# Kernel optimization log

Measured on AMD Instinct MI355X. Metric: run time of the kernel, lower is better.

Reference implementation:

```python
import jax, jax.numpy as jnp
import numpy as np

N = 1024
X_DIM = 128
Y_DIM = 128
HIDDEN = 256


def setup_inputs() -> dict:
    key = jax.random.key(0)
    ks = jax.random.split(key, 6)
    x_samples = jax.random.normal(ks[0], (N, X_DIM), dtype=jnp.float32)
    y_samples = jax.random.normal(ks[1], (N, Y_DIM), dtype=jnp.float32)
    in_dim = X_DIM + Y_DIM
    # Linear params (kaiming-uniform-ish small init)
    W1 = jax.random.normal(ks[2], (in_dim, HIDDEN), dtype=jnp.float32) / np.sqrt(in_dim)
    b1 = jnp.zeros((HIDDEN,), dtype=jnp.float32)
    W2 = jax.random.normal(ks[3], (HIDDEN, 1), dtype=jnp.float32) / np.sqrt(HIDDEN)
    b2 = jnp.zeros((1,), dtype=jnp.float32)
    return {"x_samples": x_samples, "y_samples": y_samples,
            "W1": W1, "b1": b1, "W2": W2, "b2": b2}


def reference(x_samples, y_samples, W1, b1, W2, b2):
    n = y_samples.shape[0]
    W1x, W1y = W1[:X_DIM], W1[X_DIM:]
    xp = x_samples @ W1x          # [N, H]  (x_tile[i, j] = x[j])
    yp = y_samples @ W1y          # [N, H]  (y_tile[i, j] = y[i])
    # T0: F(cat([x_i, y_i])) on the diagonal pairs -> [N, 1]
    T0 = jax.nn.relu(xp + yp + b1) @ W2 + b2
    # T1: F over all pairs (i, j) -> [N, N, 1]
    h = jax.nn.relu(yp[:, None, :] + xp[None, :, :] + b1)   # [N, N, H]
    T1 = h @ W2 + b2                                        # [N, N, 1]
    lse = jax.scipy.special.logsumexp(T1, axis=1)           # [N, 1] over dim=1
    lower_bound = T0.mean() - (lse.mean() - jnp.log(jnp.float32(n)))
    return lower_bound
```

## Files before the change

### kernel.cpp

```cpp
#include <hip/hip_runtime.h>

#define N_SAMP 1024
#define XD     128
#define HID    256


__global__ __launch_bounds__(256) void gemm_xy(
    const float* __restrict__ x, const float* __restrict__ y,
    const float* __restrict__ W1, const float* __restrict__ b1,
    float* __restrict__ xpbT, float* __restrict__ ypT,
    float* __restrict__ S, float* __restrict__ T0sum)
{
    const int k  = threadIdx.x;
    const int r0 = blockIdx.x * 4;

    if (threadIdx.x < 4) S[blockIdx.x * 4 + threadIdx.x] = 0.f;
    if (blockIdx.x == 0 && threadIdx.x == 4) T0sum[0] = 0.f;

    float ax0 = 0.f, ax1 = 0.f, ax2 = 0.f, ax3 = 0.f;
    float ay0 = 0.f, ay1 = 0.f, ay2 = 0.f, ay3 = 0.f;

    #pragma unroll 4
    for (int d = 0; d < XD; ++d) {
        const float wx = W1[d * HID + k];
        const float wy = W1[(XD + d) * HID + k];
        ax0 = fmaf(x[(r0 + 0) * XD + d], wx, ax0);
        ax1 = fmaf(x[(r0 + 1) * XD + d], wx, ax1);
        ax2 = fmaf(x[(r0 + 2) * XD + d], wx, ax2);
        ax3 = fmaf(x[(r0 + 3) * XD + d], wx, ax3);
        ay0 = fmaf(y[(r0 + 0) * XD + d], wy, ay0);
        ay1 = fmaf(y[(r0 + 1) * XD + d], wy, ay1);
        ay2 = fmaf(y[(r0 + 2) * XD + d], wy, ay2);
        ay3 = fmaf(y[(r0 + 3) * XD + d], wy, ay3);
    }

    const float bk = b1[k];
    float4 xs = make_float4(ax0 + bk, ax1 + bk, ax2 + bk, ax3 + bk);
    float4 ys = make_float4(ay0, ay1, ay2, ay3);
    *(float4*)&xpbT[k * N_SAMP + r0] = xs;
    *(float4*)&ypT [k * N_SAMP + r0] = ys;
}

__global__ __launch_bounds__(128) void pair_lse(
    const float* __restrict__ ypT, const float* __restrict__ xpbT,
    const float* __restrict__ W2,
    float* __restrict__ S, float* __restrict__ T0sum)
{
    __shared__ float yl[HID * 32];

    const int tid = threadIdx.x;
    const int tj  = tid & 15;
    const int ti  = tid >> 4;
    const int jb  = blockIdx.x * 64;
    const int ib  = blockIdx.y * 32;
    const int j0  = jb + tj * 4;
    const int i0  = ib + ti * 4;

    #pragma unroll
    for (int s = 0; s < 16; ++s) {
        const int f  = s * 128 + tid;
        const int k  = f >> 3;
        const int iq = (f & 7) * 4;
        *(float4*)&yl[k * 32 + iq] =
            *(const float4*)&ypT[k * N_SAMP + ib + iq];
    }
    __syncthreads();

    float acc[4][4];
    #pragma unroll
    for (int a = 0; a < 4; ++a)
        #pragma unroll
        for (int b = 0; b < 4; ++b) acc[a][b] = 0.f;

    const int ti4 = ti * 4;

    #pragma unroll 8
    for (int k = 0; k < HID; ++k) {
        const float4 xv = *(const float4*)&xpbT[k * N_SAMP + j0];
        const float4 yv = *(const float4*)&yl[k * 32 + ti4];
        const float  w  = W2[k];
        const float xs[4] = {xv.x, xv.y, xv.z, xv.w};
        const float ys[4] = {yv.x, yv.y, yv.z, yv.w};
        #pragma unroll
        for (int a = 0; a < 4; ++a)
            #pragma unroll
            for (int b = 0; b < 4; ++b)
                acc[a][b] = fmaf(fmaxf(ys[a] + xs[b], 0.f), w, acc[a][b]);
    }

    #pragma unroll
    for (int a = 0; a < 4; ++a) {
        float e = __expf(acc[a][0]) + __expf(acc[a][1])
                + __expf(acc[a][2]) + __expf(acc[a][3]);
        #pragma unroll
        for (int off = 8; off; off >>= 1) e += __shfl_xor(e, off, 16);
        if (tj == 0) atomicAdd(&S[i0 + a], e);
    }

    if ((int)blockIdx.x == (int)(blockIdx.y >> 1)) {
        float dv = 0.f;
        #pragma unroll
        for (int a = 0; a < 4; ++a) {
            const int dd = i0 + a - j0;
            float t = 0.f;
            if      (dd == 0) t = acc[a][0];
            else if (dd == 1) t = acc[a][1];
            else if (dd == 2) t = acc[a][2];
            else if (dd == 3) t = acc[a][3];
            dv += t;
        }
        #pragma unroll
        for (int off = 32; off; off >>= 1) dv += __shfl_xor(dv, off, 64);
        if ((tid & 63) == 0) atomicAdd(T0sum, dv);
    }
}

__global__ __launch_bounds__(256) void finalize(
    const float* __restrict__ S, const float* __restrict__ T0sum,
    const float* __restrict__ b2, float* __restrict__ out)
{
    __shared__ float red[4];
    const int tid = threadIdx.x;

    float ls = 0.f;
    for (int i = tid; i < N_SAMP; i += 256) ls += logf(S[i]);
    #pragma unroll
    for (int off = 32; off; off >>= 1) ls += __shfl_xor(ls, off, 64);
    if ((tid & 63) == 0) red[tid >> 6] = ls;
    __syncthreads();

    if (tid == 0) {
        const float lse_sum = red[0] + red[1] + red[2] + red[3];
        const float t0_mean  = T0sum[0] / (float)N_SAMP + b2[0];
        const float lse_mean = lse_sum / (float)N_SAMP + b2[0] - logf((float)N_SAMP);
        out[0] = t0_mean - lse_mean;
    }
}

extern "C" void kernel_launch(void* const* d_in, const int* in_sizes, int n_in,
                              void* d_out, int out_size, void* d_ws, size_t ws_size,
                              hipStream_t stream)
{
    const float* x  = (const float*)d_in[0];
    const float* y  = (const float*)d_in[1];
    const float* W1 = (const float*)d_in[2];
    const float* b1 = (const float*)d_in[3];
    const float* W2 = (const float*)d_in[4];
    const float* b2 = (const float*)d_in[5];

    float* ws   = (float*)d_ws;
    float* S    = ws;
    float* T0s  = ws + 1024;
    float* xpbT = ws + 2048;
    float* ypT  = ws + 2048 + HID * N_SAMP;

    gemm_xy <<<dim3(N_SAMP / 4), dim3(256), 0, stream>>>(x, y, W1, b1,
                                                         xpbT, ypT, S, T0s);
    pair_lse<<<dim3(16, 32),     dim3(128), 0, stream>>>(ypT, xpbT, W2, S, T0s);
    finalize<<<dim3(1),          dim3(256), 0, stream>>>(S, T0s, b2, (float*)d_out);
}
```

Baseline: 120.5 us.

## Split hidden dimension across blocks, stage both operands in LDS, add row LSE kernel

Result: no change. 122.5 us (+1.7%).

```diff
diff --git a/kernel.cpp b/kernel.cpp
--- a/kernel.cpp
+++ b/kernel.cpp
@@ -3,19 +3,19 @@
 #define N_SAMP 1024
 #define XD     128
 #define HID    256
+#define KHALF  128
 
 
 __global__ __launch_bounds__(256) void gemm_xy(
     const float* __restrict__ x, const float* __restrict__ y,
     const float* __restrict__ W1, const float* __restrict__ b1,
     float* __restrict__ xpbT, float* __restrict__ ypT,
-    float* __restrict__ S, float* __restrict__ T0sum)
+    float* __restrict__ T0sum)
 {
     const int k  = threadIdx.x;
     const int r0 = blockIdx.x * 4;
 
-    if (threadIdx.x < 4) S[blockIdx.x * 4 + threadIdx.x] = 0.f;
-    if (blockIdx.x == 0 && threadIdx.x == 4) T0sum[0] = 0.f;
+    if (blockIdx.x == 0 && threadIdx.x == 0) T0sum[0] = 0.f;
 
     float ax0 = 0.f, ax1 = 0.f, ax2 = 0.f, ax3 = 0.f;
     float ay0 = 0.f, ay1 = 0.f, ay2 = 0.f, ay3 = 0.f;
@@ -41,28 +41,27 @@
     *(float4*)&ypT [k * N_SAMP + r0] = ys;
 }
 
-__global__ __launch_bounds__(128) void pair_lse(
+__global__ __launch_bounds__(256) void pair_partial(
     const float* __restrict__ ypT, const float* __restrict__ xpbT,
-    const float* __restrict__ W2,
-    float* __restrict__ S, float* __restrict__ T0sum)
+    const float* __restrict__ W2, float* __restrict__ T1part)
 {
-    __shared__ float yl[HID * 32];
+    __shared__ float xs[KHALF][64];
+    __shared__ float ys[KHALF][64];
 
     const int tid = threadIdx.x;
     const int tj  = tid & 15;
     const int ti  = tid >> 4;
     const int jb  = blockIdx.x * 64;
-    const int ib  = blockIdx.y * 32;
-    const int j0  = jb + tj * 4;
-    const int i0  = ib + ti * 4;
+    const int ib  = blockIdx.y * 64;
+    const int kof = blockIdx.z * KHALF;
 
     #pragma unroll
-    for (int s = 0; s < 16; ++s) {
-        const int f  = s * 128 + tid;
-        const int k  = f >> 3;
-        const int iq = (f & 7) * 4;
-        *(float4*)&yl[k * 32 + iq] =
-            *(const float4*)&ypT[k * N_SAMP + ib + iq];
+    for (int s = 0; s < 8; ++s) {
+        const int f  = s * 256 + tid;
+        const int kk = f >> 4;
+        const int q  = (f & 15) * 4;
+        *(float4*)&xs[kk][q] = *(const float4*)&xpbT[(kof + kk) * N_SAMP + jb + q];
+        *(float4*)&ys[kk][q] = *(const float4*)&ypT [(kof + kk) * N_SAMP + ib + q];
     }
     __syncthreads();
 
@@ -72,47 +71,57 @@
         #pragma unroll
         for (int b = 0; b < 4; ++b) acc[a][b] = 0.f;
 
-    const int ti4 = ti * 4;
+    const int tj4 = tj * 4, ti4 = ti * 4;
 
     #pragma unroll 8
-    for (int k = 0; k < HID; ++k) {
-        const float4 xv = *(const float4*)&xpbT[k * N_SAMP + j0];
-        const float4 yv = *(const float4*)&yl[k * 32 + ti4];
-        const float  w  = W2[k];
-        const float xs[4] = {xv.x, xv.y, xv.z, xv.w};
-        const float ys[4] = {yv.x, yv.y, yv.z, yv.w};
+    for (int kk = 0; kk < KHALF; ++kk) {
+        const float4 xv = *(const float4*)&xs[kk][tj4];
+        const float4 yv = *(const float4*)&ys[kk][ti4];
+        const float  w  = W2[kof + kk];
+        const float xa[4] = {xv.x, xv.y, xv.z, xv.w};
+        const float ya[4] = {yv.x, yv.y, yv.z, yv.w};
         #pragma unroll
         for (int a = 0; a < 4; ++a)
             #pragma unroll
             for (int b = 0; b < 4; ++b)
-                acc[a][b] = fmaf(fmaxf(ys[a] + xs[b], 0.f), w, acc[a][b]);
+                acc[a][b] = fmaf(fmaxf(ya[a] + xa[b], 0.f), w, acc[a][b]);
     }
 
+    float* dst = T1part + ((size_t)blockIdx.z << 20);
     #pragma unroll
     for (int a = 0; a < 4; ++a) {
-        float e = __expf(acc[a][0]) + __expf(acc[a][1])
-                + __expf(acc[a][2]) + __expf(acc[a][3]);
-        #pragma unroll
-        for (int off = 8; off; off >>= 1) e += __shfl_xor(e, off, 16);
-        if (tj == 0) atomicAdd(&S[i0 + a], e);
+        float4 v = make_float4(acc[a][0], acc[a][1], acc[a][2], acc[a][3]);
+        *(float4*)&dst[(ib + ti4 + a) * N_SAMP + jb + tj4] = v;
+    }
+}
+
+__global__ __launch_bounds__(256) void row_lse(
+    const float* __restrict__ T1part,
+    float* __restrict__ S, float* __restrict__ T0sum)
+{
+    __shared__ float red[4];
+    const int i   = blockIdx.x;
+    const int tid = threadIdx.x;
+
+    const float4 a = *(const float4*)&T1part[(size_t)i * N_SAMP + tid * 4];
+    const float4 b = *(const float4*)&T1part[(1u << 20) + (size_t)i * N_SAMP + tid * 4];
+    const float t0 = a.x + b.x, t1 = a.y + b.y, t2 = a.z + b.z, t3 = a.w + b.w;
+
+    if (tid == (i >> 2)) {
+        float d;
+        if      ((i & 3) == 0) d = t0;
+        else if ((i & 3) == 1) d = t1;
+        else if ((i & 3) == 2) d = t2;
+        else                   d = t3;
+        atomicAdd(T0sum, d);
     }
 
-    if ((int)blockIdx.x == (int)(blockIdx.y >> 1)) {
-        float dv = 0.f;
-        #pragma unroll
-        for (int a = 0; a < 4; ++a) {
-            const int dd = i0 + a - j0;
-            float t = 0.f;
-            if      (dd == 0) t = acc[a][0];
-            else if (dd == 1) t = acc[a][1];
-            else if (dd == 2) t = acc[a][2];
-            else if (dd == 3) t = acc[a][3];
-            dv += t;
-        }
-        #pragma unroll
-        for (int off = 32; off; off >>= 1) dv += __shfl_xor(dv, off, 64);
-        if ((tid & 63) == 0) atomicAdd(T0sum, dv);
-    }
+    float e = __expf(t0) + __expf(t1) + __expf(t2) + __expf(t3);
+    #pragma unroll
+    for (int off = 32; off; off >>= 1) e += __shfl_xor(e, off, 64);
+    if ((tid & 63) == 0) red[tid >> 6] = e;
+    __syncthreads();
+    if (tid == 0) S[i] = red[0] + red[1] + red[2] + red[3];
 }
 
 __global__ __launch_bounds__(256) void finalize(
@@ -148,14 +157,18 @@
     const float* W2 = (const float*)d_in[4];
     const float* b2 = (const float*)d_in[5];
 
-    float* ws   = (float*)d_ws;
-    float* S    = ws;
-    float* T0s  = ws + 1024;
-    float* xpbT = ws + 2048;
-    float* ypT  = ws + 2048 + HID * N_SAMP;
+    float* ws     = (float*)d_ws;
+    float* S      = ws;
+    float* T0s    = ws + 1024;
+    float* xpbT   = ws + 2048;
+    float* ypT    = ws + 2048 + HID * N_SAMP;
+    float* T1part = ws + 2048 + 2 * HID * N_SAMP;
 
-    gemm_xy <<<dim3(N_SAMP / 4), dim3(256), 0, stream>>>(x, y, W1, b1,
-                                                         xpbT, ypT, S, T0s);
-    pair_lse<<<dim3(16, 32),     dim3(128), 0, stream>>>(ypT, xpbT, W2, S, T0s);
-    finalize<<<dim3(1),          dim3(256), 0, stream>>>(S, T0s, b2, (float*)d_out);
+    gemm_xy     <<<dim3(N_SAMP / 4),  dim3(256), 0, stream>>>(x, y, W1, b1,
+                                                              xpbT, ypT, T0s);
+    pair_partial<<<dim3(16, 16, 2),   dim3(256), 0, stream>>>(ypT, xpbT, W2,
+                                                              T1part);
+    row_lse     <<<dim3(N_SAMP),      dim3(256), 0, stream>>>(T1part, S, T0s);
+    finalize    <<<dim3(1),           dim3(256), 0, stream>>>(S, T0s, b2,
+                                                              (float*)d_out);
 }
```

## Fuse finalize into pair kernel and tile both operands in shared memory

Applied to the files above, without the earlier changes.

New measurement: 123.0 us. 2.1% more time.

```diff
diff --git a/kernel.cpp b/kernel.cpp
--- a/kernel.cpp
+++ b/kernel.cpp
@@ -16,6 +16,7 @@
 
     if (threadIdx.x < 4) S[blockIdx.x * 4 + threadIdx.x] = 0.f;
     if (blockIdx.x == 0 && threadIdx.x == 4) T0sum[0] = 0.f;
+    if (blockIdx.x == 0 && threadIdx.x == 5) ((unsigned*)T0sum)[1] = 0u;
 
     float ax0 = 0.f, ax1 = 0.f, ax2 = 0.f, ax3 = 0.f;
     float ay0 = 0.f, ay1 = 0.f, ay2 = 0.f, ay3 = 0.f;
@@ -35,36 +36,28 @@
     }
 
     const float bk = b1[k];
-    float4 xs = make_float4(ax0 + bk, ax1 + bk, ax2 + bk, ax3 + bk);
-    float4 ys = make_float4(ay0, ay1, ay2, ay3);
-    *(float4*)&xpbT[k * N_SAMP + r0] = xs;
-    *(float4*)&ypT [k * N_SAMP + r0] = ys;
+    float4 xs4 = make_float4(ax0 + bk, ax1 + bk, ax2 + bk, ax3 + bk);
+    float4 ys4 = make_float4(ay0, ay1, ay2, ay3);
+    *(float4*)&xpbT[k * N_SAMP + r0] = xs4;
+    *(float4*)&ypT [k * N_SAMP + r0] = ys4;
 }
 
-__global__ __launch_bounds__(128) void pair_lse(
+__global__ __launch_bounds__(256) void pair_fused(
     const float* __restrict__ ypT, const float* __restrict__ xpbT,
     const float* __restrict__ W2,
-    float* __restrict__ S, float* __restrict__ T0sum)
+    float* __restrict__ S, float* __restrict__ T0s,
+    const float* __restrict__ b2, float* __restrict__ out)
 {
-    __shared__ float yl[HID * 32];
+    __shared__ float xs[128][64];
+    __shared__ float ys[128][64];
 
     const int tid = threadIdx.x;
     const int tj  = tid & 15;
     const int ti  = tid >> 4;
     const int jb  = blockIdx.x * 64;
-    const int ib  = blockIdx.y * 32;
+    const int ib  = blockIdx.y * 64;
     const int j0  = jb + tj * 4;
     const int i0  = ib + ti * 4;
-
-    #pragma unroll
-    for (int s = 0; s < 16; ++s) {
-        const int f  = s * 128 + tid;
-        const int k  = f >> 3;
-        const int iq = (f & 7) * 4;
-        *(float4*)&yl[k * 32 + iq] =
-            *(const float4*)&ypT[k * N_SAMP + ib + iq];
-    }
-    __syncthreads();
 
     float acc[4][4];
     #pragma unroll
@@ -72,20 +65,33 @@
         #pragma unroll
         for (int b = 0; b < 4; ++b) acc[a][b] = 0.f;
 
-    const int ti4 = ti * 4;
+    for (int pass = 0; pass < 2; ++pass) {
+        const int kof = pass << 7;
+        if (pass) __syncthreads();
 
-    #pragma unroll 8
-    for (int k = 0; k < HID; ++k) {
-        const float4 xv = *(const float4*)&xpbT[k * N_SAMP + j0];
-        const float4 yv = *(const float4*)&yl[k * 32 + ti4];
-        const float  w  = W2[k];
-        const float xs[4] = {xv.x, xv.y, xv.z, xv.w};
-        const float ys[4] = {yv.x, yv.y, yv.z, yv.w};
         #pragma unroll
-        for (int a = 0; a < 4; ++a)
+        for (int s = 0; s < 8; ++s) {
+            const int f  = s * 256 + tid;
+            const int kk = f >> 4;
+            const int q  = (f & 15) * 4;
+            *(float4*)&xs[kk][q] = *(const float4*)&xpbT[(kof + kk) * N_SAMP + jb + q];
+            *(float4*)&ys[kk][q] = *(const float4*)&ypT [(kof + kk) * N_SAMP + ib + q];
+        }
+        __syncthreads();
+
+        #pragma unroll 8
+        for (int kk = 0; kk < 128; ++kk) {
+            const float4 xv = *(const float4*)&xs[kk][tj * 4];
+            const float4 yv = *(const float4*)&ys[kk][ti * 4];
+            const float  w  = W2[kof + kk];
+            const float xa[4] = {xv.x, xv.y, xv.z, xv.w};
+            const float ya[4] = {yv.x, yv.y, yv.z, yv.w};
             #pragma unroll
-            for (int b = 0; b < 4; ++b)
-                acc[a][b] = fmaf(fmaxf(ys[a] + xs[b], 0.f), w, acc[a][b]);
+            for (int a = 0; a < 4; ++a)
+                #pragma unroll
+                for (int b = 0; b < 4; ++b)
+                    acc[a][b] = fmaf(fmaxf(ya[a] + xa[b], 0.f), w, acc[a][b]);
+        }
     }
 
     #pragma unroll
@@ -97,42 +103,38 @@
         if (tj == 0) atomicAdd(&S[i0 + a], e);
     }
 
-    if ((int)blockIdx.x == (int)(blockIdx.y >> 1)) {
+    if (blockIdx.x == blockIdx.y) {
         float dv = 0.f;
-        #pragma unroll
-        for (int a = 0; a < 4; ++a) {
-            const int dd = i0 + a - j0;
-            float t = 0.f;
-            if      (dd == 0) t = acc[a][0];
-            else if (dd == 1) t = acc[a][1];
-            else if (dd == 2) t = acc[a][2];
-            else if (dd == 3) t = acc[a][3];
-            dv += t;
-        }
+        if (ti == tj)
+            dv = acc[0][0] + acc[1][1] + acc[2][2] + acc[3][3];
         #pragma unroll
         for (int off = 32; off; off >>= 1) dv += __shfl_xor(dv, off, 64);
-        if ((tid & 63) == 0) atomicAdd(T0sum, dv);
+        if ((tid & 63) == 0) atomicAdd(&T0s[0], dv);
     }
-}
 
-__global__ __launch_bounds__(256) void finalize(
-    const float* __restrict__ S, const float* __restrict__ T0sum,
-    const float* __restrict__ b2, float* __restrict__ out)
-{
-    __shared__ float red[4];
-    const int tid = threadIdx.x;
+    int* lastflag = (int*)&ys[0][0];
+    __threadfence();
+    __syncthreads();
+    if (tid == 0)
+        *lastflag = (atomicAdd((unsigned*)&T0s[1], 1u) == 255u);
+    __syncthreads();
+    if (!*lastflag) return;
 
+    float* red = &xs[0][0];
     float ls = 0.f;
-    for (int i = tid; i < N_SAMP; i += 256) ls += logf(S[i]);
+    for (int i = tid; i < N_SAMP; i += 256)
+        ls += logf(atomicAdd(&S[i], 0.f));
     #pragma unroll
     for (int off = 32; off; off >>= 1) ls += __shfl_xor(ls, off, 64);
     if ((tid & 63) == 0) red[tid >> 6] = ls;
     __syncthreads();
 
     if (tid == 0) {
-        const float lse_sum = red[0] + red[1] + red[2] + red[3];
-        const float t0_mean  = T0sum[0] / (float)N_SAMP + b2[0];
-        const float lse_mean = lse_sum / (float)N_SAMP + b2[0] - logf((float)N_SAMP);
+        const float t0       = atomicAdd(&T0s[0], 0.f);
+        const float lse_sum  = red[0] + red[1] + red[2] + red[3];
+        const float t0_mean  = t0 / (float)N_SAMP + b2[0];
+        const float lse_mean = lse_sum / (float)N_SAMP + b2[0]
+                             - logf((float)N_SAMP);
         out[0] = t0_mean - lse_mean;
     }
 }
@@ -154,8 +156,9 @@
     float* xpbT = ws + 2048;
     float* ypT  = ws + 2048 + HID * N_SAMP;
 
-    gemm_xy <<<dim3(N_SAMP / 4), dim3(256), 0, stream>>>(x, y, W1, b1,
-                                                         xpbT, ypT, S, T0s);
-    pair_lse<<<dim3(16, 32),     dim3(128), 0, stream>>>(ypT, xpbT, W2, S, T0s);
-    finalize<<<dim3(1),          dim3(256), 0, stream>>>(S, T0s, b2, (float*)d_out);
+    gemm_xy   <<<dim3(N_SAMP / 4), dim3(256), 0, stream>>>(x, y, W1, b1,
+                                                           xpbT, ypT, S, T0s);
+    pair_fused<<<dim3(16, 16),     dim3(256), 0, stream>>>(ypT, xpbT, W2,
+                                                           S, T0s, b2,
+                                                           (float*)d_out);
 }
```
